# Kernel optimization log

Measured on AMD Instinct MI355X. Metric: run time of the kernel, lower is better.

## Reference

```python
import jax, jax.numpy as jnp
import numpy as np

BS, H, W = 32, 768, 768


def setup_inputs() -> dict:
    key = jax.random.key(0)
    k1, k2 = jax.random.split(key)
    im = jax.random.normal(k1, (BS, 3, H, W), dtype=jnp.float32)
    flat_col = jax.random.normal(k2, (BS, 37), dtype=jnp.float32) * 0.1
    return {"im": im, "flat_col": flat_col}


def reference(im, flat_col):
    bs, c, h, w = im.shape  # c == 3
    colwarp = flat_col[:, :9].reshape(bs, 3, 3)          # per-sample 3x3 color matrix
    colshift = flat_col[:, 9:12][:, :, None, None]        # per-sample per-channel shift
    spatial = flat_col[:, 12:].reshape(bs, 1, 5, 5)       # per-sample 5x5 kernel, shared across channels

    x = im + colshift
    x = jnp.einsum('bdhw,bdc->bchw', x, colwarp)

    # Batched per-sample depthwise conv expressed as ONE grouped conv:
    # fold (batch, channel) into the feature dim and use feature_group_count = bs*3.
    k = jnp.broadcast_to(spatial, (bs, 3, 5, 5)).reshape(bs * 3, 1, 5, 5)
    xi = x.reshape(1, bs * 3, h, w)
    out = jax.lax.conv_general_dilated(
        xi, k,
        window_strides=(1, 1),
        padding=((2, 2), (2, 2)),
        dimension_numbers=('NCHW', 'OIHW', 'NCHW'),
        feature_group_count=bs * 3,
    )
    return out.reshape(bs, 3, h, w)
```

## Files before the change

kernel.cpp:

```cpp
#include <hip/hip_runtime.h>

#define NB 32
#define CH 3
#define HH 768
#define WW 768

#define TW 64
#define TH 16
#define SW 72
#define SWP 76
#define SH (TH + 4)
#define CSTRIDE (SH * SWP)
#define TPB 8
#define NTC (WW / TW)
#define NTG (HH / (TH * TPB))
#define NWG (NB * NTC * NTG)
#define UNITS (SH * (SW / 4))

typedef float v4f __attribute__((ext_vector_type(4)));

__device__ inline int pswz(int s) { return s ^ (((s >> 5) & 1) << 1); }

__global__ __launch_bounds__(256) void colwarp_conv_kernel(
    const float* __restrict__ im,
    const float* __restrict__ flat,
    float* __restrict__ out)
{
    const int d   = blockIdx.x;
    const int wid = (d & 7) * (NWG / 8) + (d >> 3);
    const int tc  = wid % NTC;
    const int t2  = wid / NTC;
    const int tg  = t2 % NTG;
    const int b   = t2 / NTG;
    const int tw0 = tc * TW;
    const int thbase = tg * (TPB * TH);

    __shared__ float xs[2][CH][SH][SWP];

    const int tid = threadIdx.x;

    const float* f = flat + b * 37;
    float Wm[3][3];
#pragma unroll
    for (int i = 0; i < 3; ++i)
#pragma unroll
        for (int j = 0; j < 3; ++j) Wm[i][j] = f[i * 3 + j];
    float sh3[3];
#pragma unroll
    for (int i = 0; i < 3; ++i) sh3[i] = f[9 + i];
    float K[5][5];
#pragma unroll
    for (int i = 0; i < 5; ++i)
#pragma unroll
        for (int j = 0; j < 5; ++j) K[i][j] = f[12 + i * 5 + j];
    float bias[3];
#pragma unroll
    for (int c = 0; c < 3; ++c)
        bias[c] = sh3[0]*Wm[0][c] + sh3[1]*Wm[1][c] + sh3[2]*Wm[2][c];

    const size_t plane = (size_t)HH * WW;
    const float* im0 = im + (size_t)b * CH * plane;

    int ur[2], uldso[2], ugw[2];
    bool uon[2], uswap[2];
#pragma unroll
    for (int ui = 0; ui < 2; ++ui) {
        const int u  = tid + 256 * ui;
        const int rr = u / (SW / 4);
        const int c4 = u - rr * (SW / 4);
        ur[ui]    = rr;
        uldso[ui] = rr * SWP + c4 * 4;
        ugw[ui]   = tw0 - 4 + c4 * 4;
        uon[ui]   = (u < UNITS);
        uswap[ui] = ((c4 >> 3) & 1) != 0;
    }

    float4 vld[2][CH];
    bool vok[2];

#define STAGE_LOAD(TH0)                                                        \
    _Pragma("unroll")                                                          \
    for (int ui = 0; ui < 2; ++ui) {                                           \
        const int gh = (TH0) + ur[ui] - 2;                                     \
        const bool ok = uon[ui] && ((unsigned)gh < (unsigned)HH)               \
                                && ((unsigned)ugw[ui] < (unsigned)WW);         \
        vok[ui] = ok;                                                          \
        if (ok) {                                                              \
            const size_t off = (size_t)gh * WW + ugw[ui];                      \
            vld[ui][0] = *(const float4*)(im0 + off);                          \
            vld[ui][1] = *(const float4*)(im0 + plane + off);                  \
            vld[ui][2] = *(const float4*)(im0 + 2 * plane + off);              \
        }                                                                      \
    }

#define STAGE_WRITE(BUFP)                                                      \
    _Pragma("unroll")                                                          \
    for (int ui = 0; ui < 2; ++ui) {                                           \
        if (uon[ui]) {                                                         \
            float4 m0 = make_float4(0.f, 0.f, 0.f, 0.f), m1 = m0, m2 = m0;     \
            if (vok[ui]) {                                                     \
                const float4 a0 = vld[ui][0], a1 = vld[ui][1], a2 = vld[ui][2];\
                m0.x = a0.x*Wm[0][0] + a1.x*Wm[1][0] + a2.x*Wm[2][0] + bias[0];\
                m0.y = a0.y*Wm[0][0] + a1.y*Wm[1][0] + a2.y*Wm[2][0] + bias[0];\
                m0.z = a0.z*Wm[0][0] + a1.z*Wm[1][0] + a2.z*Wm[2][0] + bias[0];\
                m0.w = a0.w*Wm[0][0] + a1.w*Wm[1][0] + a2.w*Wm[2][0] + bias[0];\
                m1.x = a0.x*Wm[0][1] + a1.x*Wm[1][1] + a2.x*Wm[2][1] + bias[1];\
                m1.y = a0.y*Wm[0][1] + a1.y*Wm[1][1] + a2.y*Wm[2][1] + bias[1];\
                m1.z = a0.z*Wm[0][1] + a1.z*Wm[1][1] + a2.z*Wm[2][1] + bias[1];\
                m1.w = a0.w*Wm[0][1] + a1.w*Wm[1][1] + a2.w*Wm[2][1] + bias[1];\
                m2.x = a0.x*Wm[0][2] + a1.x*Wm[1][2] + a2.x*Wm[2][2] + bias[2];\
                m2.y = a0.y*Wm[0][2] + a1.y*Wm[1][2] + a2.y*Wm[2][2] + bias[2];\
                m2.z = a0.z*Wm[0][2] + a1.z*Wm[1][2] + a2.z*Wm[2][2] + bias[2];\
                m2.w = a0.w*Wm[0][2] + a1.w*Wm[1][2] + a2.w*Wm[2][2] + bias[2];\
            }                                                                  \
            const bool sw = uswap[ui];                                         \
            const float4 w0 = sw ? make_float4(m0.z,m0.w,m0.x,m0.y) : m0;      \
            const float4 w1 = sw ? make_float4(m1.z,m1.w,m1.x,m1.y) : m1;      \
            const float4 w2 = sw ? make_float4(m2.z,m2.w,m2.x,m2.y) : m2;      \
            *(float4*)((BUFP) + 0 * CSTRIDE + uldso[ui]) = w0;                 \
            *(float4*)((BUFP) + 1 * CSTRIDE + uldso[ui]) = w1;                 \
            *(float4*)((BUFP) + 2 * CSTRIDE + uldso[ui]) = w2;                 \
        }                                                                      \
    }

    const int tx = tid & 15;
    const int ty = tid >> 4;
    const int r0 = ty;

    const int offA = pswz(4 * tx + 2);
    const int offB = pswz(4 * tx + 4);
    const int offC = pswz(4 * tx + 6);
    const int offD = pswz(4 * tx + 8);

#define CONV_STORE(BUFP, TH0)                                                  \
    {                                                                          \
        float acc[CH][4];                                                      \
        _Pragma("unroll")                                                      \
        for (int c = 0; c < CH; ++c)                                           \
            _Pragma("unroll")                                                  \
            for (int o = 0; o < 4; ++o) acc[c][o] = 0.f;                       \
        _Pragma("unroll")                                                      \
        for (int rr = 0; rr < 5; ++rr) {                                       \
            _Pragma("unroll")                                                  \
            for (int c = 0; c < CH; ++c) {                                     \
                const float* rowb = (BUFP) + c * CSTRIDE + (r0 + rr) * SWP;    \
                const float2 p0 = *(const float2*)(rowb + offA);               \
                const float2 p1 = *(const float2*)(rowb + offB);               \
                const float2 p2 = *(const float2*)(rowb + offC);               \
                const float2 p3 = *(const float2*)(rowb + offD);               \
                const float w8[8] = {p0.x, p0.y, p1.x, p1.y,                   \
                                     p2.x, p2.y, p3.x, p3.y};                  \
                _Pragma("unroll")                                              \
                for (int j = 0; j < 5; ++j) {                                  \
                    _Pragma("unroll")                                          \
                    for (int o = 0; o < 4; ++o)                                \
                        acc[c][o] += w8[o + j] * K[rr][j];                     \
                }                                                              \
            }                                                                  \
        }                                                                      \
        _Pragma("unroll")                                                      \
        for (int c = 0; c < CH; ++c) {                                         \
            float* ob = out + ((size_t)b * CH + c) * plane;                    \
            v4f vv = {acc[c][0], acc[c][1], acc[c][2], acc[c][3]};             \
            __builtin_nontemporal_store(vv,                                    \
                (v4f*)&ob[(size_t)((TH0) + r0) * WW + tw0 + tx * 4]);          \
        }                                                                      \
    }

    STAGE_LOAD(thbase);
    STAGE_WRITE(&xs[0][0][0][0]);
    __syncthreads();

#pragma unroll 1
    for (int t = 0; t < TPB; ++t) {
        const int th0 = thbase + t * TH;
        float* cur = &xs[t & 1][0][0][0];
        float* nxt = &xs[(t & 1) ^ 1][0][0][0];
        if (t + 1 < TPB) { STAGE_LOAD(th0 + TH); }
        CONV_STORE(cur, th0);
        if (t + 1 < TPB) { STAGE_WRITE(nxt); }
        __syncthreads();
    }
}

extern "C" void kernel_launch(void* const* d_in, const int* in_sizes, int n_in,
                              void* d_out, int out_size, void* d_ws, size_t ws_size,
                              hipStream_t stream) {
    const float* im   = (const float*)d_in[0];
    const float* flat = (const float*)d_in[1];
    float* out        = (float*)d_out;

    colwarp_conv_kernel<<<dim3(NWG), dim3(256), 0, stream>>>(im, flat, out);
}
```

Measured before the change: 81.10 us.

## Split workgroup into producer wave and consumer waves for staging

Adds a dedicated 64-thread producer wave per workgroup that loads the haloed input tile, applies the color matrix and writes it into the double-buffered LDS. The 256 original threads now only do the 5x5 convolution and the output stores. The aim is warp specialization, so global loads overlap with convolution instead of being interleaved in every thread's instruction stream. The cost is that one wave now does all the load work (6 units per thread, serialized in two halves), which may become the critical path each iteration. Workgroups also grow to 320 threads, which can change occupancy.

Measured after the change: 222.1 us. 174% more time.

```diff
diff --git a/kernel.cpp b/kernel.cpp
--- a/kernel.cpp
+++ b/kernel.cpp
@@ -16,12 +16,13 @@
 #define NTG (HH / (TH * TPB))
 #define NWG (NB * NTC * NTG)
 #define UNITS (SH * (SW / 4))
+#define NTHR 320
 
 typedef float v4f __attribute__((ext_vector_type(4)));
 
 __device__ inline int pswz(int s) { return s ^ (((s >> 5) & 1) << 1); }
 
-__global__ __launch_bounds__(256) void colwarp_conv_kernel(
+__global__ __launch_bounds__(NTHR) void colwarp_conv_kernel(
     const float* __restrict__ im,
     const float* __restrict__ flat,
     float* __restrict__ out)
@@ -38,6 +39,7 @@
     __shared__ float xs[2][CH][SH][SWP];
 
     const int tid = threadIdx.x;
+    const bool producer = (tid >= 256);
 
     const float* f = flat + b * 37;
     float Wm[3][3];
@@ -61,45 +63,48 @@
     const size_t plane = (size_t)HH * WW;
     const float* im0 = im + (size_t)b * CH * plane;
 
-    int ur[2], uldso[2], ugw[2];
-    bool uon[2], uswap[2];
-#pragma unroll
-    for (int ui = 0; ui < 2; ++ui) {
-        const int u  = tid + 256 * ui;
+    const int pl = tid - 256;
+    int pur[6], puldso[6], pugw[6];
+    bool puon[6], puswap[6];
+#pragma unroll
+    for (int ui = 0; ui < 6; ++ui) {
+        const int u  = (pl < 0 ? 0 : pl) + 64 * ui;
         const int rr = u / (SW / 4);
         const int c4 = u - rr * (SW / 4);
-        ur[ui]    = rr;
-        uldso[ui] = rr * SWP + c4 * 4;
-        ugw[ui]   = tw0 - 4 + c4 * 4;
-        uon[ui]   = (u < UNITS);
-        uswap[ui] = ((c4 >> 3) & 1) != 0;
-    }
-
-    float4 vld[2][CH];
-    bool vok[2];
-
-#define STAGE_LOAD(TH0)                                                        \
+        pur[ui]    = rr;
+        puldso[ui] = rr * SWP + c4 * 4;
+        pugw[ui]   = tw0 - 4 + c4 * 4;
+        puon[ui]   = (u < UNITS);
+        puswap[ui] = ((c4 >> 3) & 1) != 0;
+    }
+
+    float4 pv[3][CH];
+    bool pok[3];
+
+#define P_LOAD(BASE, TH0)                                                      \
     _Pragma("unroll")                                                          \
-    for (int ui = 0; ui < 2; ++ui) {                                           \
-        const int gh = (TH0) + ur[ui] - 2;                                     \
-        const bool ok = uon[ui] && ((unsigned)gh < (unsigned)HH)               \
-                                && ((unsigned)ugw[ui] < (unsigned)WW);         \
-        vok[ui] = ok;                                                          \
+    for (int k = 0; k < 3; ++k) {                                              \
+        const int ui = (BASE) + k;                                             \
+        const int gh = (TH0) + pur[ui] - 2;                                    \
+        const bool ok = puon[ui] && ((unsigned)gh < (unsigned)HH)              \
+                                 && ((unsigned)pugw[ui] < (unsigned)WW);       \
+        pok[k] = ok;                                                           \
         if (ok) {                                                              \
-            const size_t off = (size_t)gh * WW + ugw[ui];                      \
-            vld[ui][0] = *(const float4*)(im0 + off);                          \
-            vld[ui][1] = *(const float4*)(im0 + plane + off);                  \
-            vld[ui][2] = *(const float4*)(im0 + 2 * plane + off);              \
-        }                                                                      \
-    }
-
-#define STAGE_WRITE(BUFP)                                                      \
+            const size_t off = (size_t)gh * WW + pugw[ui];                     \
+            pv[k][0] = *(const float4*)(im0 + off);                            \
+            pv[k][1] = *(const float4*)(im0 + plane + off);                    \
+            pv[k][2] = *(const float4*)(im0 + 2 * plane + off);                \
+        }                                                                      \
+    }
+
+#define P_WRITE(BASE, BUFP)                                                    \
     _Pragma("unroll")                                                          \
-    for (int ui = 0; ui < 2; ++ui) {                                           \
-        if (uon[ui]) {                                                         \
+    for (int k = 0; k < 3; ++k) {                                              \
+        const int ui = (BASE) + k;                                             \
+        if (puon[ui]) {                                                        \
             float4 m0 = make_float4(0.f, 0.f, 0.f, 0.f), m1 = m0, m2 = m0;     \
-            if (vok[ui]) {                                                     \
-                const float4 a0 = vld[ui][0], a1 = vld[ui][1], a2 = vld[ui][2];\
+            if (pok[k]) {                                                      \
+                const float4 a0 = pv[k][0], a1 = pv[k][1], a2 = pv[k][2];      \
                 m0.x = a0.x*Wm[0][0] + a1.x*Wm[1][0] + a2.x*Wm[2][0] + bias[0];\
                 m0.y = a0.y*Wm[0][0] + a1.y*Wm[1][0] + a2.y*Wm[2][0] + bias[0];\
                 m0.z = a0.z*Wm[0][0] + a1.z*Wm[1][0] + a2.z*Wm[2][0] + bias[0];\
@@ -113,18 +118,21 @@
                 m2.z = a0.z*Wm[0][2] + a1.z*Wm[1][2] + a2.z*Wm[2][2] + bias[2];\
                 m2.w = a0.w*Wm[0][2] + a1.w*Wm[1][2] + a2.w*Wm[2][2] + bias[2];\
             }                                                                  \
-            const bool sw = uswap[ui];                                         \
+            const bool sw = puswap[ui];                                        \
             const float4 w0 = sw ? make_float4(m0.z,m0.w,m0.x,m0.y) : m0;      \
             const float4 w1 = sw ? make_float4(m1.z,m1.w,m1.x,m1.y) : m1;      \
             const float4 w2 = sw ? make_float4(m2.z,m2.w,m2.x,m2.y) : m2;      \
-            *(float4*)((BUFP) + 0 * CSTRIDE + uldso[ui]) = w0;                 \
-            *(float4*)((BUFP) + 1 * CSTRIDE + uldso[ui]) = w1;                 \
-            *(float4*)((BUFP) + 2 * CSTRIDE + uldso[ui]) = w2;                 \
-        }                                                                      \
-    }
+            *(float4*)((BUFP) + 0 * CSTRIDE + puldso[ui]) = w0;                \
+            *(float4*)((BUFP) + 1 * CSTRIDE + puldso[ui]) = w1;               \
+            *(float4*)((BUFP) + 2 * CSTRIDE + puldso[ui]) = w2;                \
+        }                                                                      \
+    }
+
+#define P_STAGE(BUFP, TH0)                                                     \
+    { P_LOAD(0, TH0); P_WRITE(0, BUFP); P_LOAD(3, TH0); P_WRITE(3, BUFP); }
 
     const int tx = tid & 15;
-    const int ty = tid >> 4;
+    const int ty = (tid >> 4) & 15;
     const int r0 = ty;
 
     const int offA = pswz(4 * tx + 2);
@@ -167,18 +175,17 @@
         }                                                                      \
     }
 
-    STAGE_LOAD(thbase);
-    STAGE_WRITE(&xs[0][0][0][0]);
+    if (producer) { P_STAGE(&xs[0][0][0][0], thbase); }
     __syncthreads();
 
 #pragma unroll 1
     for (int t = 0; t < TPB; ++t) {
         const int th0 = thbase + t * TH;
-        float* cur = &xs[t & 1][0][0][0];
-        float* nxt = &xs[(t & 1) ^ 1][0][0][0];
-        if (t + 1 < TPB) { STAGE_LOAD(th0 + TH); }
-        CONV_STORE(cur, th0);
-        if (t + 1 < TPB) { STAGE_WRITE(nxt); }
+        if (producer) {
+            if (t + 1 < TPB) { P_STAGE(&xs[(t & 1) ^ 1][0][0][0], th0 + TH); }
+        } else {
+            CONV_STORE(&xs[t & 1][0][0][0], th0);
+        }
         __syncthreads();
     }
 }
@@ -190,5 +197,5 @@
     const float* flat = (const float*)d_in[1];
     float* out        = (float*)d_out;
 
-    colwarp_conv_kernel<<<dim3(NWG), dim3(256), 0, stream>>>(im, flat, out);
+    colwarp_conv_kernel<<<dim3(NWG), dim3(NTHR), 0, stream>>>(im, flat, out);
 }
```
